# Performance work log

Measured on AMD Instinct MI355X. Metric: run time of the kernel, lower is better.

## Reference

```python
import jax, jax.numpy as jnp
import numpy as np

M, C, K, D = 2048, 16, 8, 256  # queries, classes, clusters/class, feature_dim
H1, H2 = D, D // 2             # MLP hidden sizes


def setup_inputs() -> dict:
    key = jax.random.key(0)
    ks = jax.random.split(key, 8)
    s1 = 1.0 / np.sqrt(2 * D)
    s2 = 1.0 / np.sqrt(H1)
    s3 = 1.0 / np.sqrt(H2)
    return {
        "query_features": jax.random.normal(ks[0], (M, D), jnp.float32),
        "prototypes": jax.random.normal(ks[1], (C, K, D), jnp.float32),
        "W1": jax.random.normal(ks[2], (2 * D, H1), jnp.float32) * s1,
        "b1": jnp.zeros((H1,), jnp.float32),
        "W2": jax.random.normal(ks[3], (H1, H2), jnp.float32) * s2,
        "b2": jnp.zeros((H2,), jnp.float32),
        "W3": jax.random.normal(ks[4], (H2, 1), jnp.float32) * s3,
        "b3": jnp.zeros((1,), jnp.float32),
    }


def reference(query_features, prototypes, W1, b1, W2, b2, W3, b3):
    # Attention MLP on concat([query, prototype]) for every (query, class, cluster)
    # pair. Split W1 into the query half and prototype half so we never
    # materialize the [M,C,K,2D] concat; broadcast-add instead.
    d = query_features.shape[-1]
    Wq, Wp = W1[:d], W1[d:]
    qh = query_features @ Wq                      # [M, H1]
    ph = jnp.einsum('ckd,dh->ckh', prototypes, Wp)  # [C, K, H1]
    h = jax.nn.relu(qh[:, None, None, :] + ph[None] + b1)   # [M, C, K, H1]
    h = jax.nn.relu(h @ W2 + b2)                              # [M, C, K, H2]
    scores = (h @ W3)[..., 0] + b3[0]                         # [M, C, K]
    attn = jax.nn.softmax(scores, axis=-1)                    # softmax over clusters
    weighted = jnp.einsum('mck,ckd->mcd', attn, prototypes)   # [M, C, D]
    diff = query_features[:, None, :] - weighted              # [M, C, D]
    distances = jnp.sqrt(jnp.sum(diff * diff, axis=-1))       # [M, C]
    return -distances
```

## Files before the change

### kernel.cpp

```cpp
#include <hip/hip_runtime.h>
#include <hip/hip_fp16.h>
#include <cstdint>

typedef __attribute__((ext_vector_type(8))) _Float16 f16x8;
typedef __attribute__((ext_vector_type(4))) float f32x4;
typedef __attribute__((ext_vector_type(16))) float f32x16;

__device__ __forceinline__ f16x8 cvt8(float4 x, float4 y) {
    f16x8 r;
    r[0] = (_Float16)x.x; r[1] = (_Float16)x.y; r[2] = (_Float16)x.z; r[3] = (_Float16)x.w;
    r[4] = (_Float16)y.x; r[5] = (_Float16)y.y; r[6] = (_Float16)y.z; r[7] = (_Float16)y.w;
    return r;
}

__device__ __forceinline__ f16x8 relu8(f16x8 v) {
    f16x8 z = {};
    return __builtin_elementwise_max(v, z);
}

__global__ __launch_bounds__(256)
void xpose(const float* __restrict__ query,
           const float* __restrict__ prot,
           const float* __restrict__ W1,
           const float* __restrict__ W2,
           const float* __restrict__ b2,
           _Float16* __restrict__ w1t,
           f16x8* __restrict__ w2p,
           float* __restrict__ Gm,
           float* __restrict__ q2) {
    int b = blockIdx.x, t = threadIdx.x;
    if (b < 32) {
        __shared__ _Float16 lt[64][73];
        int bi = b >> 2, bj = b & 3;
        int r0 = bi * 64, c0 = bj * 64;
        #pragma unroll
        for (int it = 0; it < 4; ++it) {
            int row = it * 16 + (t >> 4);
            int c4 = (t & 15) * 4;
            float4 v = *(const float4*)(W1 + (r0 + row) * 256 + c0 + c4);
            lt[row][c4]     = (_Float16)v.x;
            lt[row][c4 + 1] = (_Float16)v.y;
            lt[row][c4 + 2] = (_Float16)v.z;
            lt[row][c4 + 3] = (_Float16)v.w;
        }
        __syncthreads();
        int c = t >> 2, kq = t & 3;
        unsigned short o[16];
        #pragma unroll
        for (int i = 0; i < 16; ++i) {
            union { _Float16 f; unsigned short s; } u;
            u.f = lt[kq * 16 + i][c];
            o[i] = u.s;
        }
        _Float16* dst = w1t + (r0 >= 256 ? 65536 : 0) + (c0 + c) * 256 + (r0 & 255) + kq * 16;
        *(uint4*)dst       = *(uint4*)&o[0];
        *(uint4*)(dst + 8) = *(uint4*)&o[8];
    } else if (b < 49) {
        int chunk = (b - 32) * 256 + t;
        int ks = chunk >> 8, h = (chunk >> 7) & 1, c = chunk & 127;
        f16x8 o = {};
        if (ks < 16) {
            #pragma unroll
            for (int j = 0; j < 8; ++j)
                o[j] = (_Float16)W2[(ks * 16 + h * 8 + j) * 128 + c];
        } else if (h == 0) {
            o[0] = (_Float16)b2[c];
        }
        w2p[chunk] = o;
    } else if (b < 81) {
        int pid = (b - 49) * 32 + (t >> 3), l8 = t & 7;
        int c = pid >> 6, k = (pid >> 3) & 7, kp = pid & 7;
        const float4* pa = (const float4*)(prot + (c * 8 + k) * 256 + l8 * 32);
        const float4* pb = (const float4*)(prot + (c * 8 + kp) * 256 + l8 * 32);
        float s = 0.f;
        #pragma unroll
        for (int i = 0; i < 8; ++i) {
            float4 x = pa[i], y = pb[i];
            s += x.x * y.x + x.y * y.y + x.z * y.z + x.w * y.w;
        }
        s += __shfl_xor(s, 1); s += __shfl_xor(s, 2); s += __shfl_xor(s, 4);
        if (l8 == 0) Gm[pid] = s;
    } else {
        int m = (b - 81) * 32 + (t >> 3), l8 = t & 7;
        const float4* qp = (const float4*)(query + m * 256 + l8 * 32);
        float s = 0.f;
        #pragma unroll
        for (int i = 0; i < 8; ++i) {
            float4 x = qp[i];
            s += x.x * x.x + x.y * x.y + x.z * x.z + x.w * x.w;
        }
        s += __shfl_xor(s, 1); s += __shfl_xor(s, 2); s += __shfl_xor(s, 4);
        if (l8 == 0) q2[m] = s;
    }
}

__global__ __launch_bounds__(256, 2)
void prepg(const float* __restrict__ query,
           const float* __restrict__ prot,
           const _Float16* __restrict__ w1t,
           const float* __restrict__ b1,
           _Float16* __restrict__ qh16,
           float* __restrict__ sqp,
           _Float16* __restrict__ phpk) {
    int b = blockIdx.x, t = threadIdx.x;
    int w = t >> 6, l = t & 63, l15 = l & 15, l4 = l >> 4;
    int mode, row0, col0;
    if (b < 128)      { mode = 0; row0 = (b >> 2) * 64;         col0 = (b & 3) * 64; }
    else if (b < 192) { mode = 1; row0 = ((b - 128) >> 1) * 64; col0 = ((b - 128) & 1) * 64; }
    else              { mode = 2; row0 = ((b - 192) >> 2) * 64; col0 = ((b - 192) & 3) * 64; }
    const float* Asrc = (mode == 2) ? prot : query;
    const _Float16* Bsrc = (mode == 2) ? (w1t + 65536) : w1t;

    f32x4 acc[4];
    #pragma unroll
    for (int nt = 0; nt < 4; ++nt) acc[nt] = (f32x4){0.f, 0.f, 0.f, 0.f};

    for (int ks = 0; ks < 8; ++ks) {
        int row = row0 + w * 16 + l15;
        const float* ap = Asrc + row * 256 + ks * 32 + l4 * 8;
        f16x8 af = cvt8(*(const float4*)ap, *(const float4*)(ap + 4));
        f16x8 bf[4];
        #pragma unroll
        for (int nt = 0; nt < 4; ++nt) {
            int col = col0 + nt * 16 + l15;
            if (mode == 1) {
                const float* bp = prot + col * 256 + ks * 32 + l4 * 8;
                bf[nt] = cvt8(*(const float4*)bp, *(const float4*)(bp + 4));
            } else {
                bf[nt] = *(const f16x8*)(Bsrc + col * 256 + ks * 32 + l4 * 8);
            }
        }
        #pragma unroll
        for (int nt = 0; nt < 4; ++nt)
            acc[nt] = __builtin_amdgcn_mfma_f32_16x16x32_f16(af, bf[nt], acc[nt], 0, 0, 0);
    }
    #pragma unroll
    for (int nt = 0; nt < 4; ++nt)
        #pragma unroll
        for (int j = 0; j < 4; ++j) {
            int row = row0 + w * 16 + l4 * 4 + j;
            int col = col0 + nt * 16 + l15;
            float v = acc[nt][j];
            if (mode == 0)      qh16[row * 256 + col] = (_Float16)v;
            else if (mode == 1) sqp[row * 128 + col] = v;
            else                phpk[(((col >> 4) * 2 + ((col >> 3) & 1)) * 128 + row) * 8
                                     + (col & 7)] = (_Float16)(v + b1[col]);
        }
}

__global__ __launch_bounds__(512, 1)
void fused4(const _Float16* __restrict__ qh16,
            const uint4* __restrict__ phpk,
            const uint4* __restrict__ w2p,
            const float* __restrict__ sqp,
            const float* __restrict__ q2,
            const float* __restrict__ Gm,
            const float* __restrict__ W3,
            float* __restrict__ out) {
    __shared__ _Float16 qlds[16 * 256];
    __shared__ float w3l[128];
    __shared__ float spart[2][2][4][64];

    int t = threadIdx.x;
    int wid = t >> 6, l = t & 63;
    int rg = wid & 1, cs = wid >> 1;
    int lk = l & 31, h = l >> 5;
    int ch = blockIdx.x & 1;
    int mg = blockIdx.x >> 1;
    int ckl = rg * 32 + lk;
    int ck = ch * 64 + ckl;
    int m0 = mg * 16;

    const _Float16* w2h = (const _Float16*)w2p;
    const _Float16* phh = (const _Float16*)phpk;

    ((uint4*)qlds)[t] = ((const uint4*)(qh16 + m0 * 256))[t];
    if (t < 128) w3l[t] = W3[t];

    f16x8 wA[17];
    #pragma unroll
    for (int ks = 0; ks < 17; ++ks)
        wA[ks] = *(const f16x8*)(w2h + ((ks * 2 + h) * 128 + cs * 32 + lk) * 8);

    f16x8 ph[16];
    #pragma unroll
    for (int ks = 0; ks < 16; ++ks)
        ph[ks] = *(const f16x8*)(phh + ((ks * 2 + h) * 128 + ck) * 8);

    __syncthreads();

    for (int mi = 0; mi < 8; ++mi) {
        int mA = m0 + mi * 2;
        const _Float16* qra = qlds + (mi * 2) * 256 + h * 8;
        const _Float16* qrb = qra + 256;

        f32x16 accA = {}, accB = {};

        f16x8 qa[2], qb[2];
        qa[0] = *(const f16x8*)(qra);       qb[0] = *(const f16x8*)(qrb);
        qa[1] = *(const f16x8*)(qra + 16);  qb[1] = *(const f16x8*)(qrb + 16);

        #pragma unroll
        for (int ks = 0; ks < 16; ++ks) {
            f16x8 aA = relu8(qa[ks & 1] + ph[ks]);
            f16x8 aB = relu8(qb[ks & 1] + ph[ks]);
            if (ks < 14) {
                qa[ks & 1] = *(const f16x8*)(qra + (ks + 2) * 16);
                qb[ks & 1] = *(const f16x8*)(qrb + (ks + 2) * 16);
            }
            accA = __builtin_amdgcn_mfma_f32_32x32x16_f16(wA[ks], aA, accA, 0, 0, 0);
            accB = __builtin_amdgcn_mfma_f32_32x32x16_f16(wA[ks], aB, accB, 0, 0, 0);
        }
        {
            f16x8 e = {};
            if (h == 0) e[0] = (_Float16)1.0f;
            accA = __builtin_amdgcn_mfma_f32_32x32x16_f16(wA[16], e, accA, 0, 0, 0);
            accB = __builtin_amdgcn_mfma_f32_32x32x16_f16(wA[16], e, accB, 0, 0, 0);
        }

        int buf = mi & 1;
        {
            float s0 = 0.f, s1 = 0.f, s2 = 0.f, s3 = 0.f;
            #pragma unroll
            for (int r = 0; r < 16; r += 4) {
                s0 = fmaf(fmaxf(accA[r + 0], 0.f), w3l[cs * 32 + ((r + 0) & 3) + 8 * ((r + 0) >> 2) + 4 * h], s0);
                s1 = fmaf(fmaxf(accA[r + 1], 0.f), w3l[cs * 32 + ((r + 1) & 3) + 8 * ((r + 1) >> 2) + 4 * h], s1);
                s2 = fmaf(fmaxf(accA[r + 2], 0.f), w3l[cs * 32 + ((r + 2) & 3) + 8 * ((r + 2) >> 2) + 4 * h], s2);
                s3 = fmaf(fmaxf(accA[r + 3], 0.f), w3l[cs * 32 + ((r + 3) & 3) + 8 * ((r + 3) >> 2) + 4 * h], s3);
            }
            float s = (s0 + s1) + (s2 + s3);
            s += __shfl_xor(s, 32);
            if (l < 32) spart[buf][0][cs][ckl] = s;
        }
        {
            float s0 = 0.f, s1 = 0.f, s2 = 0.f, s3 = 0.f;
            #pragma unroll
            for (int r = 0; r < 16; r += 4) {
                s0 = fmaf(fmaxf(accB[r + 0], 0.f), w3l[cs * 32 + ((r + 0) & 3) + 8 * ((r + 0) >> 2) + 4 * h], s0);
                s1 = fmaf(fmaxf(accB[r + 1], 0.f), w3l[cs * 32 + ((r + 1) & 3) + 8 * ((r + 1) >> 2) + 4 * h], s1);
                s2 = fmaf(fmaxf(accB[r + 2], 0.f), w3l[cs * 32 + ((r + 2) & 3) + 8 * ((r + 2) >> 2) + 4 * h], s2);
                s3 = fmaf(fmaxf(accB[r + 3], 0.f), w3l[cs * 32 + ((r + 3) & 3) + 8 * ((r + 3) >> 2) + 4 * h], s3);
            }
            float s = (s0 + s1) + (s2 + s3);
            s += __shfl_xor(s, 32);
            if (l < 32) spart[buf][1][cs][ckl] = s;
        }
        __syncthreads();

        if (t < 128) {
            int msel = t >> 6, cl = t & 63, kk = t & 7;
            int m = mA + msel;
            int cg = ch * 8 + (cl >> 3);
            float s = spart[buf][msel][0][cl] + spart[buf][msel][1][cl]
                    + spart[buf][msel][2][cl] + spart[buf][msel][3][cl];
            float mx = s;
            mx = fmaxf(mx, __shfl_xor(mx, 1));
            mx = fmaxf(mx, __shfl_xor(mx, 2));
            mx = fmaxf(mx, __shfl_xor(mx, 4));
            float e = __expf(s - mx);
            float den = e;
            den += __shfl_xor(den, 1); den += __shfl_xor(den, 2); den += __shfl_xor(den, 4);
            float a = e / den;
            float p2 = a * sqp[m * 128 + ch * 64 + cl];
            float p3 = 0.f;
            #pragma unroll
            for (int kq = 0; kq < 8; ++kq) {
                float ak = __shfl(a, (l & 56) | kq);
                p3 = fmaf(ak, Gm[cg * 64 + kq * 8 + kk], p3);
            }
            p3 *= a;
            float pr = p3 - 2.f * p2;
            pr += __shfl_xor(pr, 1); pr += __shfl_xor(pr, 2); pr += __shfl_xor(pr, 4);
            if (kk == 0)
                out[m * 16 + cg] = -sqrtf(fmaxf(q2[m] + pr, 0.f));
        }
    }
}

extern "C" void kernel_launch(void* const* d_in, const int* in_sizes, int n_in,
                              void* d_out, int out_size, void* d_ws, size_t ws_size,
                              hipStream_t stream) {
    const float* query = (const float*)d_in[0];
    const float* prot  = (const float*)d_in[1];
    const float* W1    = (const float*)d_in[2];
    const float* b1    = (const float*)d_in[3];
    const float* W2    = (const float*)d_in[4];
    const float* b2    = (const float*)d_in[5];
    const float* W3    = (const float*)d_in[6];

    char* ws = (char*)d_ws;
    _Float16* qh16 = (_Float16*)(ws);
    _Float16* w1t  = (_Float16*)(ws + 1048576);
    f16x8*    w2p  = (f16x8*)(ws + 1310720);
    _Float16* phpk = (_Float16*)(ws + 1380352);
    float*    sqp  = (float*)(ws + 1445888);
    float*    q2   = (float*)(ws + 2494464);
    float*    Gm   = (float*)(ws + 2502656);
    float* out = (float*)d_out;

    xpose<<<145, 256, 0, stream>>>(query, prot, W1, W2, b2, w1t, w2p, Gm, q2);
    prepg<<<200, 256, 0, stream>>>(query, prot, w1t, b1, qh16, sqp, phpk);
    fused4<<<256, 512, 0, stream>>>(qh16, (const uint4*)phpk, (const uint4*)w2p,
                                    sqp, q2, Gm, W3, out);
}
```

Baseline: 42.78 us.

## Merge W1 transpose into GEMM prep kernel via per-block LDS transpose

Removes the separate xpose kernel and its w1t workspace. Each GEMM block of the merged prep kernel now loads its 256x64 slice of W1 from global memory, converts it to fp16 and transposes it into LDS before the MFMA loop. The small auxiliary jobs (w2p packing, Gm, q2) run as extra blocks of the same launch. This saves one kernel launch and a global round-trip, at the cost of redundant W1 loads across row blocks (each W1 slice is reloaded by 32 blocks) and higher LDS use per block.

```diff
diff --git a/kernel.cpp b/kernel.cpp
--- a/kernel.cpp
+++ b/kernel.cpp
@@ -18,45 +18,84 @@
     return __builtin_elementwise_max(v, z);
 }
 
-__global__ __launch_bounds__(256)
-void xpose(const float* __restrict__ query,
+__global__ __launch_bounds__(256, 2)
+void prep1(const float* __restrict__ query,
            const float* __restrict__ prot,
            const float* __restrict__ W1,
+           const float* __restrict__ b1,
            const float* __restrict__ W2,
            const float* __restrict__ b2,
-           _Float16* __restrict__ w1t,
+           _Float16* __restrict__ qh16,
+           float* __restrict__ sqp,
+           _Float16* __restrict__ phpk,
            f16x8* __restrict__ w2p,
            float* __restrict__ Gm,
            float* __restrict__ q2) {
+    __shared__ _Float16 Bls[64][280];
     int b = blockIdx.x, t = threadIdx.x;
-    if (b < 32) {
-        __shared__ _Float16 lt[64][73];
-        int bi = b >> 2, bj = b & 3;
-        int r0 = bi * 64, c0 = bj * 64;
-        #pragma unroll
-        for (int it = 0; it < 4; ++it) {
-            int row = it * 16 + (t >> 4);
-            int c4 = (t & 15) * 4;
-            float4 v = *(const float4*)(W1 + (r0 + row) * 256 + c0 + c4);
-            lt[row][c4]     = (_Float16)v.x;
-            lt[row][c4 + 1] = (_Float16)v.y;
-            lt[row][c4 + 2] = (_Float16)v.z;
-            lt[row][c4 + 3] = (_Float16)v.w;
-        }
-        __syncthreads();
-        int c = t >> 2, kq = t & 3;
-        unsigned short o[16];
-        #pragma unroll
-        for (int i = 0; i < 16; ++i) {
-            union { _Float16 f; unsigned short s; } u;
-            u.f = lt[kq * 16 + i][c];
-            o[i] = u.s;
-        }
-        _Float16* dst = w1t + (r0 >= 256 ? 65536 : 0) + (c0 + c) * 256 + (r0 & 255) + kq * 16;
-        *(uint4*)dst       = *(uint4*)&o[0];
-        *(uint4*)(dst + 8) = *(uint4*)&o[8];
-    } else if (b < 49) {
-        int chunk = (b - 32) * 256 + t;
+
+    if (b < 200) {
+        int mode, row0, col0;
+        if (b < 128)      { mode = 0; row0 = (b >> 2) * 64;         col0 = (b & 3) * 64; }
+        else if (b < 192) { mode = 1; row0 = ((b - 128) >> 1) * 64; col0 = ((b - 128) & 1) * 64; }
+        else              { mode = 2; row0 = ((b - 192) >> 2) * 64; col0 = ((b - 192) & 3) * 64; }
+        const float* Asrc = (mode == 2) ? prot : query;
+
+        if (mode != 1) {
+            int woff = (mode == 2) ? 256 : 0;
+            int rr = t >> 4, c4 = (t & 15) * 4;
+            for (int rt = 0; rt < 4; ++rt) {
+                #pragma unroll
+                for (int it = 0; it < 4; ++it) {
+                    int k = rt * 64 + it * 16 + rr;
+                    float4 v = *(const float4*)(W1 + (woff + k) * 256 + col0 + c4);
+                    Bls[c4 + 0][k] = (_Float16)v.x;
+                    Bls[c4 + 1][k] = (_Float16)v.y;
+                    Bls[c4 + 2][k] = (_Float16)v.z;
+                    Bls[c4 + 3][k] = (_Float16)v.w;
+                }
+            }
+            __syncthreads();
+        }
+
+        int w = t >> 6, l = t & 63, l15 = l & 15, l4 = l >> 4;
+        f32x4 acc[4];
+        #pragma unroll
+        for (int nt = 0; nt < 4; ++nt) acc[nt] = (f32x4){0.f, 0.f, 0.f, 0.f};
+
+        for (int ks = 0; ks < 8; ++ks) {
+            int row = row0 + w * 16 + l15;
+            const float* ap = Asrc + row * 256 + ks * 32 + l4 * 8;
+            f16x8 af = cvt8(*(const float4*)ap, *(const float4*)(ap + 4));
+            f16x8 bf[4];
+            #pragma unroll
+            for (int nt = 0; nt < 4; ++nt) {
+                if (mode == 1) {
+                    int col = col0 + nt * 16 + l15;
+                    const float* bp = prot + col * 256 + ks * 32 + l4 * 8;
+                    bf[nt] = cvt8(*(const float4*)bp, *(const float4*)(bp + 4));
+                } else {
+                    bf[nt] = *(const f16x8*)(&Bls[nt * 16 + l15][ks * 32 + l4 * 8]);
+                }
+            }
+            #pragma unroll
+            for (int nt = 0; nt < 4; ++nt)
+                acc[nt] = __builtin_amdgcn_mfma_f32_16x16x32_f16(af, bf[nt], acc[nt], 0, 0, 0);
+        }
+        #pragma unroll
+        for (int nt = 0; nt < 4; ++nt)
+            #pragma unroll
+            for (int j = 0; j < 4; ++j) {
+                int row = row0 + w * 16 + l4 * 4 + j;
+                int col = col0 + nt * 16 + l15;
+                float v = acc[nt][j];
+                if (mode == 0)      qh16[row * 256 + col] = (_Float16)v;
+                else if (mode == 1) sqp[row * 128 + col] = v;
+                else                phpk[(((col >> 4) * 2 + ((col >> 3) & 1)) * 128 + row) * 8
+                                         + (col & 7)] = (_Float16)(v + b1[col]);
+            }
+    } else if (b < 217) {
+        int chunk = (b - 200) * 256 + t;
         int ks = chunk >> 8, h = (chunk >> 7) & 1, c = chunk & 127;
         f16x8 o = {};
         if (ks < 16) {
@@ -67,8 +106,8 @@
             o[0] = (_Float16)b2[c];
         }
         w2p[chunk] = o;
-    } else if (b < 81) {
-        int pid = (b - 49) * 32 + (t >> 3), l8 = t & 7;
+    } else if (b < 249) {
+        int pid = (b - 217) * 32 + (t >> 3), l8 = t & 7;
         int c = pid >> 6, k = (pid >> 3) & 7, kp = pid & 7;
         const float4* pa = (const float4*)(prot + (c * 8 + k) * 256 + l8 * 32);
         const float4* pb = (const float4*)(prot + (c * 8 + kp) * 256 + l8 * 32);
@@ -81,7 +120,7 @@
         s += __shfl_xor(s, 1); s += __shfl_xor(s, 2); s += __shfl_xor(s, 4);
         if (l8 == 0) Gm[pid] = s;
     } else {
-        int m = (b - 81) * 32 + (t >> 3), l8 = t & 7;
+        int m = (b - 249) * 32 + (t >> 3), l8 = t & 7;
         const float4* qp = (const float4*)(query + m * 256 + l8 * 32);
         float s = 0.f;
         #pragma unroll
@@ -92,60 +131,6 @@
         s += __shfl_xor(s, 1); s += __shfl_xor(s, 2); s += __shfl_xor(s, 4);
         if (l8 == 0) q2[m] = s;
     }
-}
-
-__global__ __launch_bounds__(256, 2)
-void prepg(const float* __restrict__ query,
-           const float* __restrict__ prot,
-           const _Float16* __restrict__ w1t,
-           const float* __restrict__ b1,
-           _Float16* __restrict__ qh16,
-           float* __restrict__ sqp,
-           _Float16* __restrict__ phpk) {
-    int b = blockIdx.x, t = threadIdx.x;
-    int w = t >> 6, l = t & 63, l15 = l & 15, l4 = l >> 4;
-    int mode, row0, col0;
-    if (b < 128)      { mode = 0; row0 = (b >> 2) * 64;         col0 = (b & 3) * 64; }
-    else if (b < 192) { mode = 1; row0 = ((b - 128) >> 1) * 64; col0 = ((b - 128) & 1) * 64; }
-    else              { mode = 2; row0 = ((b - 192) >> 2) * 64; col0 = ((b - 192) & 3) * 64; }
-    const float* Asrc = (mode == 2) ? prot : query;
-    const _Float16* Bsrc = (mode == 2) ? (w1t + 65536) : w1t;
-
-    f32x4 acc[4];
-    #pragma unroll
-    for (int nt = 0; nt < 4; ++nt) acc[nt] = (f32x4){0.f, 0.f, 0.f, 0.f};
-
-    for (int ks = 0; ks < 8; ++ks) {
-        int row = row0 + w * 16 + l15;
-        const float* ap = Asrc + row * 256 + ks * 32 + l4 * 8;
-        f16x8 af = cvt8(*(const float4*)ap, *(const float4*)(ap + 4));
-        f16x8 bf[4];
-        #pragma unroll
-        for (int nt = 0; nt < 4; ++nt) {
-            int col = col0 + nt * 16 + l15;
-            if (mode == 1) {
-                const float* bp = prot + col * 256 + ks * 32 + l4 * 8;
-                bf[nt] = cvt8(*(const float4*)bp, *(const float4*)(bp + 4));
-            } else {
-                bf[nt] = *(const f16x8*)(Bsrc + col * 256 + ks * 32 + l4 * 8);
-            }
-        }
-        #pragma unroll
-        for (int nt = 0; nt < 4; ++nt)
-            acc[nt] = __builtin_amdgcn_mfma_f32_16x16x32_f16(af, bf[nt], acc[nt], 0, 0, 0);
-    }
-    #pragma unroll
-    for (int nt = 0; nt < 4; ++nt)
-        #pragma unroll
-        for (int j = 0; j < 4; ++j) {
-            int row = row0 + w * 16 + l4 * 4 + j;
-            int col = col0 + nt * 16 + l15;
-            float v = acc[nt][j];
-            if (mode == 0)      qh16[row * 256 + col] = (_Float16)v;
-            else if (mode == 1) sqp[row * 128 + col] = v;
-            else                phpk[(((col >> 4) * 2 + ((col >> 3) & 1)) * 128 + row) * 8
-                                     + (col & 7)] = (_Float16)(v + b1[col]);
-        }
 }
 
 __global__ __launch_bounds__(512, 1)
@@ -290,16 +275,15 @@
 
     char* ws = (char*)d_ws;
     _Float16* qh16 = (_Float16*)(ws);
-    _Float16* w1t  = (_Float16*)(ws + 1048576);
-    f16x8*    w2p  = (f16x8*)(ws + 1310720);
-    _Float16* phpk = (_Float16*)(ws + 1380352);
-    float*    sqp  = (float*)(ws + 1445888);
-    float*    q2   = (float*)(ws + 2494464);
-    float*    Gm   = (float*)(ws + 2502656);
+    f16x8*    w2p  = (f16x8*)(ws + 1048576);
+    _Float16* phpk = (_Float16*)(ws + 1118208);
+    float*    sqp  = (float*)(ws + 1183744);
+    float*    q2   = (float*)(ws + 2232320);
+    float*    Gm   = (float*)(ws + 2240512);
     float* out = (float*)d_out;
 
-    xpose<<<145, 256, 0, stream>>>(query, prot, W1, W2, b2, w1t, w2p, Gm, q2);
-    prepg<<<200, 256, 0, stream>>>(query, prot, w1t, b1, qh16, sqp, phpk);
+    prep1<<<313, 256, 0, stream>>>(query, prot, W1, b1, W2, b2,
+                                   qh16, sqp, phpk, w2p, Gm, q2);
     fused4<<<256, 512, 0, stream>>>(qh16, (const uint4*)phpk, (const uint4*)w2p,
                                     sqp, q2, Gm, W3, out);
 }
```

Result: faster. 39.46 us, median of 2 (-7.8%).
